# Optimization experiments

Measured on AMD Instinct MI355X. Metric: run time of the kernel, lower is better.

Reference implementation:

```python
import jax, jax.numpy as jnp
import numpy as np


def _conv3(x, w):
    # 3x3 conv, stride 1, padding 1 (SAME), NCHW/OIHW
    return jax.lax.conv_general_dilated(
        x, w, window_strides=(1, 1), padding=((1, 1), (1, 1)),
        dimension_numbers=("NCHW", "OIHW", "NCHW"))


def setup_inputs() -> dict:
    key = jax.random.key(0)
    ks = jax.random.split(key, 10)
    B, C, H, W = 16, 64, 128, 128
    NL = 4
    inp = {
        "x0": jax.random.normal(ks[0], (B, C, H, W), dtype=jnp.float32),
        "spa_mask": jax.random.uniform(ks[1], (B, 1, H, W), dtype=jnp.float32),
        # uniform noise in (0,1) for gumbel; bounded away from 0 like the torch retry loop
        "gumbels": jax.random.uniform(ks[2], (1, C, NL, 2), dtype=jnp.float32,
                                      minval=1e-6, maxval=1.0 - 1e-6),
        "ch_mask_param": jax.random.uniform(ks[3], (1, C, NL, 2), dtype=jnp.float32),
        "w0": jax.random.normal(ks[4], (C, C, 3, 3), dtype=jnp.float32) * 0.05,
        "w1": jax.random.normal(ks[5], (C, C, 3, 3), dtype=jnp.float32) * 0.05,
        "w2": jax.random.normal(ks[6], (C, C, 3, 3), dtype=jnp.float32) * 0.05,
        "w3": jax.random.normal(ks[7], (C, C, 3, 3), dtype=jnp.float32) * 0.05,
        "wc": jax.random.normal(ks[8], (C, C * NL, 1, 1), dtype=jnp.float32) * 0.05,
        "bc": jax.random.normal(ks[9], (C,), dtype=jnp.float32) * 0.05,
    }
    return inp


def reference(x0, spa_mask, gumbels, ch_mask_param, w0, w1, w2, w3, wc, bc):
    tau = 1.0
    g = -jnp.log(-jnp.log(gumbels))
    ch_mask = jax.nn.softmax((ch_mask_param + g) / tau, axis=3)  # (1,C,NL,2)
    ws = [w0, w1, w2, w3]
    outs = []
    fea = x0
    for i in range(4):
        m_d = ch_mask[:, :, i, 0][:, :, None, None]  # dense-path channel gate (1,C,1,1)
        m_s = ch_mask[:, :, i, 1][:, :, None, None]  # sparse-path channel gate
        if i == 0:
            fea = _conv3(fea, ws[0])
            fea = fea * m_s * spa_mask + fea * m_d
        else:
            fea_d = _conv3(fea * m_d, ws[i])
            fea_s = _conv3(fea * m_s, ws[i])
            fea = (fea_d * m_s * spa_mask + fea_d * m_d
                   + fea_s * m_s * spa_mask + fea_s * m_d * spa_mask)
        fea = jax.nn.relu(fea)
        outs.append(fea)
    cat = jnp.concatenate(outs, axis=1)  # (B, 4C, H, W)
    out = jnp.einsum("oc,bchw->bohw", wc[:, :, 0, 0], cat) + bc[None, :, None, None]
    return (out, ch_mask)
```

## Files before the change

### kernel.cpp

```cpp
#include <hip/hip_runtime.h>
#include <math.h>

#define B_ 16
#define C_ 64
#define H_ 128
#define W_ 128
#define HW_ (H_*W_)
#define OUT_ELEMS 16777216

#define CHM_B    0
#define PWA_B    2048
#define AH_B     34816
#define FEA_B(s) (550912u + (size_t)(s)*33554432u)

#define A_S0   0
#define A_S(s) (36864 + ((s)-1)*73728)

typedef __attribute__((ext_vector_type(4))) short  v4s;
typedef __attribute__((ext_vector_type(8))) short  v8s;
typedef __attribute__((ext_vector_type(4))) float  v4f;

__device__ __forceinline__ ushort f2bf(float f) {
    unsigned u = __builtin_bit_cast(unsigned, f);
    unsigned r = u + 0x7FFFu + ((u >> 16) & 1u);
    return (ushort)(r >> 16);
}
__device__ __forceinline__ v8s ld_b64x2(const ushort* p) {
    v4s a = *(const v4s*)(const void*)p;
    v4s b = *(const v4s*)(const void*)(p + 4);
    return __builtin_shufflevector(a, b, 0, 1, 2, 3, 4, 5, 6, 7);
}

__global__ __launch_bounds__(64) void mask_kernel(
    const float* __restrict__ gum, const float* __restrict__ par,
    float* __restrict__ chm, float* __restrict__ out_tail)
{
    int c = threadIdx.x;
    #pragma unroll
    for (int i = 0; i < 4; ++i) {
        int base = (c*4 + i)*2;
        float g0 = -logf(-logf(gum[base]));
        float g1 = -logf(-logf(gum[base+1]));
        float a0 = par[base] + g0, a1 = par[base+1] + g1;
        float mx = fmaxf(a0, a1);
        float e0 = expf(a0 - mx), e1 = expf(a1 - mx);
        float inv = 1.0f / (e0 + e1);
        float m0 = e0*inv, m1 = e1*inv;
        chm[base] = m0; chm[base+1] = m1;
        out_tail[base] = m0; out_tail[base+1] = m1;
    }
}

__global__ __launch_bounds__(256) void prep_kernel(
    const float* __restrict__ w0, const float* __restrict__ w1,
    const float* __restrict__ w2, const float* __restrict__ w3,
    const float* __restrict__ wc, const float* __restrict__ chm,
    ushort* __restrict__ AH, ushort* __restrict__ pwA)
{
    int idx = blockIdx.x*256 + threadIdx.x;
    if (idx < 36864) {
        int blk = idx >> 11;
        int r3  = idx & 2047;
        int oc = r3 >> 5, icl = r3 & 31;
        int cc = blk / 9, t = blk - 9*cc;
        int ic = cc*32 + icl;
        AH[idx] = f2bf(w0[(oc*64 + ic)*9 + t]);
    } else if (idx < 258048) {
        int j = idx - 36864;
        int s = 1 + j / 73728;
        int r = j % 73728;
        int blk = r >> 12;
        int r3  = r & 4095;
        int ocM = r3 >> 5, icl = r3 & 31;
        int cc = blk / 9, t = blk - 9*cc;
        int ic = cc*32 + icl;
        int oc = ocM >> 1, set = ocM & 1;
        const float* wsrc = (s == 1) ? w1 : (s == 2 ? w2 : w3);
        AH[idx] = f2bf(wsrc[(oc*64 + ic)*9 + t] * chm[(ic*4 + s)*2 + set]);
    } else {
        int r = idx - 258048;
        pwA[r] = f2bf(wc[r]);
    }
}

template<int NSETS, bool INF32>
__global__ __launch_bounds__(256, 2) void conv_bf16(
    const void* __restrict__ inv, const ushort* __restrict__ A,
    const float* __restrict__ chm, const float* __restrict__ spa,
    ushort* __restrict__ feaOut, int stage)
{
    constexpr int MOC = 64*NSETS;
    constexpr int MT  = MOC/32;
    __shared__ __align__(16) ushort sB[3*130*36];

    const int tid  = threadIdx.x;
    const int lane = tid & 63, wave = tid >> 6;
    const int wrow = wave >> 1, wcol = wave & 1;
    const int q = lane >> 4, ln16 = lane & 15;
    const int h = blockIdx.x & 127, b = blockIdx.x >> 7;

    {
        v8s z = (v8s){0,0,0,0,0,0,0,0};
        for (int e = tid; e < 1755; e += 256)
            *(v8s*)(void*)(sB + e*8) = z;
    }

    v4f acc[MT][4];
    #pragma unroll
    for (int m = 0; m < MT; ++m)
        #pragma unroll
        for (int n = 0; n < 4; ++n) acc[m][n] = (v4f){0.f, 0.f, 0.f, 0.f};

    int aRow[MT];
    #pragma unroll
    for (int m = 0; m < MT; ++m)
        aRow[m] = (wrow*(MOC/2) + m*16 + ln16)*32 + q*8;

    for (int c = 0; c < 2; ++c) {
        const int ic0 = c*32;
        __syncthreads();
        {
            v8s stg[6];
            #pragma unroll
            for (int it = 0; it < 6; ++it) {
                int i  = it*256 + tid;
                int ry = i >> 9;
                int r  = i & 511;
                int ic = r >> 4, wv = r & 15;
                int gh = h - 1 + ry;
                v8s v = (v8s){0,0,0,0,0,0,0,0};
                if ((unsigned)gh < 128u) {
                    size_t gi = (size_t)((b*C_ + ic0 + ic)*H_ + gh)*W_ + wv*8;
                    if constexpr (INF32) {
                        const float* s = (const float*)inv + gi;
                        v4f a0 = *(const v4f*)(const void*)s;
                        v4f a1 = *(const v4f*)(const void*)(s + 4);
                        #pragma unroll
                        for (int j = 0; j < 4; ++j) {
                            v[j]   = (short)f2bf(a0[j]);
                            v[4+j] = (short)f2bf(a1[j]);
                        }
                    } else {
                        v = *(const v8s*)(const void*)((const ushort*)inv + gi);
                    }
                }
                stg[it] = v;
            }
            #pragma unroll
            for (int it = 0; it < 6; ++it) {
                int i  = it*256 + tid;
                int ry = i >> 9;
                int r  = i & 511;
                int ic = r >> 4, wv = r & 15;
                ushort* dst = &sB[(ry*130 + wv*8 + 1)*36 + ic];
                #pragma unroll
                for (int j = 0; j < 8; ++j) dst[j*36] = (ushort)stg[it][j];
            }
        }
        __syncthreads();

        const ushort* Ab = A + c*9*MOC*32;
        v8s af[MT];
        #pragma unroll
        for (int m = 0; m < MT; ++m)
            af[m] = *(const v8s*)(const void*)(Ab + aRow[m]);

        #pragma unroll
        for (int t = 0; t < 9; ++t) {
            v8s afn[MT];
            if (t < 8) {
                #pragma unroll
                for (int m = 0; m < MT; ++m)
                    afn[m] = *(const v8s*)(const void*)(Ab + (t+1)*MOC*32 + aRow[m]);
            }
            const int ky = t/3, kx = t - 3*(t/3);
            #pragma unroll
            for (int nt = 0; nt < 4; ++nt) {
                int col = wcol*64 + nt*16 + ln16 + kx;
                v8s bf = ld_b64x2(&sB[(ky*130 + col)*36 + q*8]);
                #pragma unroll
                for (int m = 0; m < MT; ++m)
                    acc[m][nt] = __builtin_amdgcn_mfma_f32_16x16x32_bf16(af[m], bf, acc[m][nt], 0, 0, 0);
            }
            if (t < 8) {
                #pragma unroll
                for (int m = 0; m < MT; ++m) af[m] = afn[m];
            }
        }
    }

    const float* spaRow = &spa[b*HW_ + h*W_];
    #pragma unroll
    for (int nt = 0; nt < 4; ++nt) {
        int px = wcol*64 + nt*16 + ln16;
        float sp = spaRow[px];
        #pragma unroll
        for (int m = 0; m < MT; ++m) {
            if constexpr (NSETS == 2) {
                #pragma unroll
                for (int rp = 0; rp < 2; ++rp) {
                    int oc = wrow*32 + m*8 + q*2 + rp;
                    float md = chm[(oc*4 + stage)*2 + 0];
                    float ms = chm[(oc*4 + stage)*2 + 1];
                    float f = acc[m][nt][2*rp]*(ms*sp + md)
                            + acc[m][nt][2*rp+1]*((ms + md)*sp);
                    feaOut[((size_t)(b*C_ + oc)*H_ + h)*W_ + px] = f2bf(fmaxf(f, 0.f));
                }
            } else {
                #pragma unroll
                for (int r = 0; r < 4; ++r) {
                    int oc = wrow*32 + m*16 + q*4 + r;
                    float md = chm[(oc*4 + stage)*2 + 0];
                    float ms = chm[(oc*4 + stage)*2 + 1];
                    float f = acc[m][nt][r]*(ms*sp + md);
                    feaOut[((size_t)(b*C_ + oc)*H_ + h)*W_ + px] = f2bf(fmaxf(f, 0.f));
                }
            }
        }
    }
}

__global__ __launch_bounds__(256, 2) void pw_final(
    const ushort* __restrict__ fea, const ushort* __restrict__ pwA,
    const float* __restrict__ bc, float* __restrict__ out)
{
    __shared__ __align__(16) ushort sF[64*260];

    const int tid  = threadIdx.x;
    const int lane = tid & 63, wave = tid >> 6;
    const int wrow = wave >> 1, wcol = wave & 1;
    const int q = lane >> 4, ln16 = lane & 15;
    const int half = blockIdx.x & 1;
    const int h = (blockIdx.x >> 1) & 127;
    const int b = blockIdx.x >> 8;
    const int px0 = half*64;

    {
        v8s stg[8];
        #pragma unroll
        for (int it = 0; it < 8; ++it) {
            int i  = it*256 + tid;
            int s  = i >> 9;
            int r  = i & 511;
            int ic = r >> 3, pxv = r & 7;
            stg[it] = *(const v8s*)(const void*)(
                fea + (size_t)s*OUT_ELEMS + ((size_t)(b*C_ + ic)*H_ + h)*W_ + px0 + pxv*8);
        }
        #pragma unroll
        for (int it = 0; it < 8; ++it) {
            int i  = it*256 + tid;
            int s  = i >> 9;
            int r  = i & 511;
            int ic = r >> 3, pxv = r & 7;
            ushort* dst = &sF[(pxv*8)*260 + s*64 + ic];
            #pragma unroll
            for (int j = 0; j < 8; ++j) dst[j*260] = (ushort)stg[it][j];
        }
    }
    __syncthreads();

    v4f acc[2][2];
    #pragma unroll
    for (int m = 0; m < 2; ++m)
        #pragma unroll
        for (int n = 0; n < 2; ++n) acc[m][n] = (v4f){0.f, 0.f, 0.f, 0.f};

    #pragma unroll
    for (int ks = 0; ks < 8; ++ks) {
        v8s a[2];
        #pragma unroll
        for (int m = 0; m < 2; ++m)
            a[m] = *(const v8s*)(const void*)(pwA + (wrow*32 + m*16 + ln16)*256 + ks*32 + q*8);
        #pragma unroll
        for (int n = 0; n < 2; ++n) {
            int px = wcol*32 + n*16 + ln16;
            v8s bf = ld_b64x2(&sF[px*260 + ks*32 + q*8]);
            #pragma unroll
            for (int m = 0; m < 2; ++m)
                acc[m][n] = __builtin_amdgcn_mfma_f32_16x16x32_bf16(a[m], bf, acc[m][n], 0, 0, 0);
        }
    }

    #pragma unroll
    for (int n = 0; n < 2; ++n) {
        int px = px0 + wcol*32 + n*16 + ln16;
        #pragma unroll
        for (int m = 0; m < 2; ++m)
            #pragma unroll
            for (int r = 0; r < 4; ++r) {
                int o = wrow*32 + m*16 + q*4 + r;
                out[((size_t)(b*C_ + o)*H_ + h)*W_ + px] = acc[m][n][r] + bc[o];
            }
    }
}

extern "C" void kernel_launch(void* const* d_in, const int* in_sizes, int n_in,
                              void* d_out, int out_size, void* d_ws, size_t ws_size,
                              hipStream_t stream)
{
    const float* x0  = (const float*)d_in[0];
    const float* spa = (const float*)d_in[1];
    const float* gum = (const float*)d_in[2];
    const float* par = (const float*)d_in[3];
    const float* w0  = (const float*)d_in[4];
    const float* w1  = (const float*)d_in[5];
    const float* w2  = (const float*)d_in[6];
    const float* w3  = (const float*)d_in[7];
    const float* wc  = (const float*)d_in[8];
    const float* bc  = (const float*)d_in[9];
    float* out = (float*)d_out;
    char*  ws  = (char*)d_ws;

    float*  chm = (float*)(ws + CHM_B);
    ushort* pwA = (ushort*)(ws + PWA_B);
    ushort* AH  = (ushort*)(ws + AH_B);
    ushort* fea0 = (ushort*)(ws + FEA_B(0));
    ushort* fea1 = (ushort*)(ws + FEA_B(1));
    ushort* fea2 = (ushort*)(ws + FEA_B(2));
    ushort* fea3 = (ushort*)(ws + FEA_B(3));

    mask_kernel<<<1, 64, 0, stream>>>(gum, par, chm, out + OUT_ELEMS);
    prep_kernel<<<1072, 256, 0, stream>>>(w0, w1, w2, w3, wc, chm, AH, pwA);

    conv_bf16<1, true ><<<2048, 256, 0, stream>>>(x0,   AH + A_S0,  chm, spa, fea0, 0);
    conv_bf16<2, false><<<2048, 256, 0, stream>>>(fea0, AH + A_S(1), chm, spa, fea1, 1);
    conv_bf16<2, false><<<2048, 256, 0, stream>>>(fea1, AH + A_S(2), chm, spa, fea2, 2);
    conv_bf16<2, false><<<2048, 256, 0, stream>>>(fea2, AH + A_S(3), chm, spa, fea3, 3);

    pw_final<<<4096, 256, 0, stream>>>(fea0, pwA, bc, out);
}
```

Baseline: 437.6 us.

## Prefetch second input-channel half during compute, swizzle LDS, remap blocks

The conv kernel now issues global loads for the second 32-channel half before computing on the first half, so memory latency overlaps MFMA work. The weight-fragment prefetch is deepened to two taps ahead. An XOR swizzle is added to the LDS layout in both the conv and pointwise kernels to cut bank conflicts on the strided scatter stores and reads. Block indices are permuted across (b,h) so neighbouring blocks are spread out. Together these raise register pressure, which could hurt occupancy under launch_bounds(256,2).

```diff
diff --git a/kernel.cpp b/kernel.cpp
--- a/kernel.cpp
+++ b/kernel.cpp
@@ -97,7 +97,8 @@
     const int lane = tid & 63, wave = tid >> 6;
     const int wrow = wave >> 1, wcol = wave & 1;
     const int q = lane >> 4, ln16 = lane & 15;
-    const int h = blockIdx.x & 127, b = blockIdx.x >> 7;
+    const int wk = (blockIdx.x & 7)*256 + (blockIdx.x >> 3);
+    const int h = wk & 127, b = wk >> 7;
 
     {
         v8s z = (v8s){0,0,0,0,0,0,0,0};
@@ -116,78 +117,100 @@
     for (int m = 0; m < MT; ++m)
         aRow[m] = (wrow*(MOC/2) + m*16 + ln16)*32 + q*8;
 
-    for (int c = 0; c < 2; ++c) {
-        const int ic0 = c*32;
-        __syncthreads();
-        {
-            v8s stg[6];
-            #pragma unroll
-            for (int it = 0; it < 6; ++it) {
-                int i  = it*256 + tid;
-                int ry = i >> 9;
-                int r  = i & 511;
-                int ic = r >> 4, wv = r & 15;
-                int gh = h - 1 + ry;
+    v8s stgA[6], stgB[6];
+    v4f stgAF[12], stgBF[12];
+
+    auto issue = [&](int ic0, v8s* stg, v4f* stgF) {
+        #pragma unroll
+        for (int it = 0; it < 6; ++it) {
+            int i  = it*256 + tid;
+            int ry = i >> 9;
+            int r  = i & 511;
+            int ic = r >> 4, wv = r & 15;
+            int gh = h - 1 + ry;
+            if constexpr (INF32) {
+                v4f a0 = (v4f){0.f,0.f,0.f,0.f}, a1 = a0;
+                if ((unsigned)gh < 128u) {
+                    const float* s = (const float*)inv +
+                        ((size_t)((b*C_ + ic0 + ic)*H_ + gh)*W_ + wv*8);
+                    a0 = *(const v4f*)(const void*)s;
+                    a1 = *(const v4f*)(const void*)(s + 4);
+                }
+                stgF[it*2] = a0; stgF[it*2+1] = a1;
+            } else {
                 v8s v = (v8s){0,0,0,0,0,0,0,0};
-                if ((unsigned)gh < 128u) {
-                    size_t gi = (size_t)((b*C_ + ic0 + ic)*H_ + gh)*W_ + wv*8;
-                    if constexpr (INF32) {
-                        const float* s = (const float*)inv + gi;
-                        v4f a0 = *(const v4f*)(const void*)s;
-                        v4f a1 = *(const v4f*)(const void*)(s + 4);
-                        #pragma unroll
-                        for (int j = 0; j < 4; ++j) {
-                            v[j]   = (short)f2bf(a0[j]);
-                            v[4+j] = (short)f2bf(a1[j]);
-                        }
-                    } else {
-                        v = *(const v8s*)(const void*)((const ushort*)inv + gi);
-                    }
+                if ((unsigned)gh < 128u)
+                    v = *(const v8s*)(const void*)((const ushort*)inv +
+                        ((size_t)((b*C_ + ic0 + ic)*H_ + gh)*W_ + wv*8));
+                stg[it] = v;
+            }
+        }
+    };
+    auto scatter = [&](const v8s* stg, const v4f* stgF) {
+        #pragma unroll
+        for (int it = 0; it < 6; ++it) {
+            int i  = it*256 + tid;
+            int ry = i >> 9;
+            int r  = i & 511;
+            int ic = r >> 4, wv = r & 15;
+            int colBase = ry*130 + wv*8 + 1;
+            ushort vals[8];
+            if constexpr (INF32) {
+                #pragma unroll
+                for (int j = 0; j < 4; ++j) {
+                    vals[j]   = f2bf(stgF[it*2][j]);
+                    vals[4+j] = f2bf(stgF[it*2+1][j]);
                 }
-                stg[it] = v;
-            }
-            #pragma unroll
-            for (int it = 0; it < 6; ++it) {
-                int i  = it*256 + tid;
-                int ry = i >> 9;
-                int r  = i & 511;
-                int ic = r >> 4, wv = r & 15;
-                ushort* dst = &sB[(ry*130 + wv*8 + 1)*36 + ic];
-                #pragma unroll
-                for (int j = 0; j < 8; ++j) dst[j*36] = (ushort)stg[it][j];
-            }
-        }
-        __syncthreads();
-
-        const ushort* Ab = A + c*9*MOC*32;
-        v8s af[MT];
+            } else {
+                #pragma unroll
+                for (int j = 0; j < 8; ++j) vals[j] = (ushort)stg[it][j];
+            }
+            #pragma unroll
+            for (int j = 0; j < 8; ++j) {
+                int colIdx = colBase + j;
+                sB[colIdx*36 + (ic ^ (((colIdx >> 3) & 3) << 3))] = vals[j];
+            }
+        }
+    };
+    auto compute = [&](const ushort* Ab) {
+        v8s af0[MT], af1[MT], af2[MT];
         #pragma unroll
         for (int m = 0; m < MT; ++m)
-            af[m] = *(const v8s*)(const void*)(Ab + aRow[m]);
-
+            af0[m] = *(const v8s*)(const void*)(Ab + aRow[m]);
+        #pragma unroll
+        for (int m = 0; m < MT; ++m)
+            af1[m] = *(const v8s*)(const void*)(Ab + MOC*32 + aRow[m]);
         #pragma unroll
         for (int t = 0; t < 9; ++t) {
-            v8s afn[MT];
-            if (t < 8) {
+            if (t < 7) {
                 #pragma unroll
                 for (int m = 0; m < MT; ++m)
-                    afn[m] = *(const v8s*)(const void*)(Ab + (t+1)*MOC*32 + aRow[m]);
+                    af2[m] = *(const v8s*)(const void*)(Ab + (t+2)*MOC*32 + aRow[m]);
             }
             const int ky = t/3, kx = t - 3*(t/3);
             #pragma unroll
             for (int nt = 0; nt < 4; ++nt) {
-                int col = wcol*64 + nt*16 + ln16 + kx;
-                v8s bf = ld_b64x2(&sB[(ky*130 + col)*36 + q*8]);
+                int colIdx = ky*130 + wcol*64 + nt*16 + ln16 + kx;
+                v8s bf = ld_b64x2(&sB[colIdx*36 + ((q ^ ((colIdx >> 3) & 3)) << 3)]);
                 #pragma unroll
                 for (int m = 0; m < MT; ++m)
-                    acc[m][nt] = __builtin_amdgcn_mfma_f32_16x16x32_bf16(af[m], bf, acc[m][nt], 0, 0, 0);
-            }
-            if (t < 8) {
-                #pragma unroll
-                for (int m = 0; m < MT; ++m) af[m] = afn[m];
-            }
-        }
-    }
+                    acc[m][nt] = __builtin_amdgcn_mfma_f32_16x16x32_bf16(af0[m], bf, acc[m][nt], 0, 0, 0);
+            }
+            #pragma unroll
+            for (int m = 0; m < MT; ++m) { af0[m] = af1[m]; af1[m] = af2[m]; }
+        }
+    };
+
+    issue(0, stgA, stgAF);
+    __syncthreads();
+    scatter(stgA, stgAF);
+    issue(32, stgB, stgBF);
+    __syncthreads();
+    compute(A);
+    __syncthreads();
+    scatter(stgB, stgBF);
+    __syncthreads();
+    compute(A + 9*MOC*32);
 
     const float* spaRow = &spa[b*HW_ + h*W_];
     #pragma unroll
@@ -252,7 +275,8 @@
             int s  = i >> 9;
             int r  = i & 511;
             int ic = r >> 3, pxv = r & 7;
-            ushort* dst = &sF[(pxv*8)*260 + s*64 + ic];
+            int kS = (s*64 + ic) ^ ((pxv & 3) << 3);
+            ushort* dst = &sF[(pxv*8)*260 + kS];
             #pragma unroll
             for (int j = 0; j < 8; ++j) dst[j*260] = (ushort)stg[it][j];
         }
@@ -274,7 +298,8 @@
         #pragma unroll
         for (int n = 0; n < 2; ++n) {
             int px = wcol*32 + n*16 + ln16;
-            v8s bf = ld_b64x2(&sF[px*260 + ks*32 + q*8]);
+            int swz = (px >> 3) & 3;
+            v8s bf = ld_b64x2(&sF[px*260 + ks*32 + ((q ^ swz) << 3)]);
             #pragma unroll
             for (int m = 0; m < 2; ++m)
                 acc[m][n] = __builtin_amdgcn_mfma_f32_16x16x32_bf16(a[m], bf, acc[m][n], 0, 0, 0);
```

Result: faster. 426.8 us (-2.5%).
